# Kernel optimization log

Hardware: AMD Instinct MI355X
Metric: run time of the kernel (lower is better)

The kernel has to match this reference:

```python
import jax, jax.numpy as jnp
import numpy as np

N = 100000
E = 1600000
D_IN = 128
D_H = 128
D_OUT = 40


def setup_inputs() -> dict:
    key = jax.random.key(0)
    ks = jax.random.split(key, 16)
    x = jax.random.normal(ks[0], (N, D_IN), dtype=jnp.float32)
    edge_src = jax.random.randint(ks[1], (E,), 0, N, dtype=jnp.int32)
    edge_dst = jax.random.randint(ks[2], (E,), 0, N, dtype=jnp.int32)

    def glorot(k, shape):
        fan_in, fan_out = shape[1], shape[0]
        lim = jnp.sqrt(6.0 / (fan_in + fan_out)).astype(jnp.float32)
        return jax.random.uniform(k, shape, jnp.float32, -lim, lim)

    # SAGEConv params: Wl acts on aggregated neighbors, Wr on root, plus bias.
    Wl0 = glorot(ks[3], (D_H, D_IN)); Wr0 = glorot(ks[4], (D_H, D_IN)); b0 = jnp.zeros((D_H,), jnp.float32)
    Wl1 = glorot(ks[5], (D_H, D_H));  Wr1 = glorot(ks[6], (D_H, D_H));  b1 = jnp.zeros((D_H,), jnp.float32)
    Wl2 = glorot(ks[7], (D_OUT, D_H)); Wr2 = glorot(ks[8], (D_OUT, D_H)); b2 = jnp.zeros((D_OUT,), jnp.float32)
    return {"x": x, "edge_src": edge_src, "edge_dst": edge_dst,
            "Wl0": Wl0, "Wr0": Wr0, "b0": b0,
            "Wl1": Wl1, "Wr1": Wr1, "b1": b1,
            "Wl2": Wl2, "Wr2": Wr2, "b2": b2}


def _mean_aggregate(x, edge_src, edge_dst, inv_deg):
    # adj_t @ x with mean reduce: sum neighbor feats into dst, divide by degree
    agg = jax.ops.segment_sum(x[edge_src], edge_dst, num_segments=N)
    return agg * inv_deg


def _sage_conv(x, edge_src, edge_dst, inv_deg, Wl, Wr, b):
    agg = _mean_aggregate(x, edge_src, edge_dst, inv_deg)
    return agg @ Wl.T + x @ Wr.T + b


def reference(x, edge_src, edge_dst, Wl0, Wr0, b0, Wl1, Wr1, b1, Wl2, Wr2, b2):
    deg = jax.ops.segment_sum(jnp.ones((E,), jnp.float32), edge_dst, num_segments=N)
    inv_deg = (1.0 / jnp.maximum(deg, 1.0))[:, None]  # [N,1]
    h = _sage_conv(x, edge_src, edge_dst, inv_deg, Wl0, Wr0, b0)
    h = jax.nn.relu(h)  # dropout is identity in eval mode
    h = _sage_conv(h, edge_src, edge_dst, inv_deg, Wl1, Wr1, b1)
    h = jax.nn.relu(h)
    h = _sage_conv(h, edge_src, edge_dst, inv_deg, Wl2, Wr2, b2)
    return jax.nn.log_softmax(h, axis=-1)
```

## Files before the change

kernel.cpp:

```cpp
#include <hip/hip_runtime.h>
#include <hip/hip_fp16.h>
#include <math.h>

#define NN 100000
#define NE 1600000
#define D 128
#define DOUT 40
#define NBUCK 391
#define CHUNK 4096
#define NCHUNK 391
#define EPT 16
#define LSTR 136
#define BCAP 5120

typedef _Float16 half8v __attribute__((ext_vector_type(8)));
typedef __attribute__((ext_vector_type(4))) float f32x4;

__device__ __forceinline__ unsigned packh(float a, float b) {
  return (unsigned)__half_as_ushort(__float2half_rn(a)) |
         ((unsigned)__half_as_ushort(__float2half_rn(b)) << 16);
}
__device__ __forceinline__ unsigned char f2fp8(float v) {
  return (unsigned char)(__builtin_amdgcn_cvt_pk_fp8_f32(v, v, 0, 0) & 0xff);
}
#define CVT2(u, s) __builtin_amdgcn_cvt_pk_f32_fp8((int)(u), s)
#define ACCR(v) { auto q = CVT2((v).x, 0); a[0] += q[0]; a[1] += q[1];   \
  q = CVT2((v).x, 1); a[2] += q[0];  a[3] += q[1];                        \
  q = CVT2((v).y, 0); a[4] += q[0];  a[5] += q[1];                        \
  q = CVT2((v).y, 1); a[6] += q[0];  a[7] += q[1];                        \
  q = CVT2((v).z, 0); a[8] += q[0];  a[9] += q[1];                        \
  q = CVT2((v).z, 1); a[10] += q[0]; a[11] += q[1];                       \
  q = CVT2((v).w, 0); a[12] += q[0]; a[13] += q[1];                       \
  q = CVT2((v).w, 1); a[14] += q[0]; a[15] += q[1]; }
#define ACCR8(v) { auto q = CVT2((v).x, 0); a[0] += q[0]; a[1] += q[1];  \
  q = CVT2((v).x, 1); a[2] += q[0]; a[3] += q[1];                         \
  q = CVT2((v).y, 0); a[4] += q[0]; a[5] += q[1];                         \
  q = CVT2((v).y, 1); a[6] += q[0]; a[7] += q[1]; }

__global__ __launch_bounds__(256) void prep_all_kernel(
    const float* __restrict__ x, _Float16* __restrict__ xb, unsigned char* __restrict__ x8,
    const float* __restrict__ Wl0, const float* __restrict__ Wr0, half8v* __restrict__ B0,
    const float* __restrict__ Wl1, const float* __restrict__ Wr1, half8v* __restrict__ B1,
    const float* __restrict__ Wl2, const float* __restrict__ Wr2, half8v* __restrict__ By2,
    int* __restrict__ bucket_cnt) {
  int bid = blockIdx.x;
  int t = threadIdx.x;
  if (bid < 6250) {
    int i = (bid * 256 + t) * 8;
    float4 v0 = *(const float4*)(x + i);
    float4 v1 = *(const float4*)(x + i + 4);
    uint4 oh;
    oh.x = packh(v0.x, v0.y);
    oh.y = packh(v0.z, v0.w);
    oh.z = packh(v1.x, v1.y);
    oh.w = packh(v1.z, v1.w);
    *(uint4*)(xb + i) = oh;
    unsigned w0 = __builtin_amdgcn_cvt_pk_fp8_f32(v0.x, v0.y, 0, 0);
    w0 = __builtin_amdgcn_cvt_pk_fp8_f32(v0.z, v0.w, w0, 1);
    unsigned w1 = __builtin_amdgcn_cvt_pk_fp8_f32(v1.x, v1.y, 0, 0);
    w1 = __builtin_amdgcn_cvt_pk_fp8_f32(v1.z, v1.w, w1, 1);
    *(uint2*)(x8 + i) = make_uint2(w0, w1);
  } else if (bid < 6282) {
    const float* Wl = (bid < 6266) ? Wl0 : Wl1;
    const float* Wr = (bid < 6266) ? Wr0 : Wr1;
    half8v* P = (bid < 6266) ? B0 : B1;
    int rel = (bid < 6266) ? bid - 6250 : bid - 6266;
    int ob = rel * 4 + (t >> 6);
    int l = t & 63;
    int s = ob >> 3, n = ob & 7;
    int k0 = s * 32 + (l >> 4) * 8;
    int c = n * 16 + (l & 15);
    const float* W = (k0 < 128) ? Wl : Wr;
    int kb = (k0 < 128) ? k0 : k0 - 128;
    half8v h;
#pragma unroll
    for (int i = 0; i < 8; ++i) h[i] = (_Float16)W[c * 128 + kb + i];
    P[ob * 64 + l] = h;
  } else if (bid < 6287) {
    int rel = bid - 6282;
    int ob = rel * 4 + (t >> 6);
    int l = t & 63;
    int s = ob / 5, n = ob % 5;
    int k0 = s * 32 + (l >> 4) * 8;
    int c = n * 16 + (l & 15);
    const float* W = (c < DOUT) ? Wl2 : Wr2;
    int row = (c < DOUT) ? c : c - DOUT;
    half8v h;
#pragma unroll
    for (int i = 0; i < 8; ++i) h[i] = (_Float16)W[row * 128 + k0 + i];
    By2[ob * 64 + l] = h;
  } else {
    for (int i = t; i < NBUCK; i += 256) bucket_cnt[i] = 0;
  }
}

__global__ __launch_bounds__(256) void bucket_hist_kernel(const int* __restrict__ dst,
                                                          int* __restrict__ bucket_cnt) {
  __shared__ int bc[NBUCK];
  int t = threadIdx.x;
  for (int i = t; i < NBUCK; i += 256) bc[i] = 0;
  __syncthreads();
  int e_base = blockIdx.x * CHUNK;
#pragma unroll
  for (int j = 0; j < EPT; ++j) {
    int e = e_base + j * 256 + t;
    if (e < NE) atomicAdd(&bc[dst[e] >> 8], 1);
  }
  __syncthreads();
  for (int i = t; i < NBUCK; i += 256)
    if (bc[i]) atomicAdd(&bucket_cnt[i], bc[i]);
}

__global__ __launch_bounds__(512) void bucket_scan_kernel(const int* __restrict__ bucket_cnt,
                                                          int* __restrict__ bucket_base,
                                                          int* __restrict__ bucket_cursor) {
  __shared__ int s[512];
  int t = threadIdx.x;
  int c = (t < NBUCK) ? bucket_cnt[t] : 0;
  s[t] = c;
  __syncthreads();
  for (int off = 1; off < 512; off <<= 1) {
    int v = (t >= off) ? s[t - off] : 0;
    __syncthreads();
    s[t] += v;
    __syncthreads();
  }
  if (t < NBUCK) {
    int b = s[t] - c;
    bucket_base[t] = b;
    bucket_cursor[t] = b;
  }
  if (t == NBUCK) bucket_base[NBUCK] = s[NBUCK - 1];
}

__global__ __launch_bounds__(256) void binned_scatter_kernel(const int* __restrict__ src,
                                                             const int* __restrict__ dst,
                                                             int* __restrict__ bucket_cursor,
                                                             unsigned* __restrict__ pairs) {
  __shared__ int lcnt[NBUCK];
  __shared__ int lscan[NBUCK];
  __shared__ int gb[NBUCK];
  __shared__ unsigned ebuf[CHUNK];
  __shared__ unsigned short bbuf[CHUNK];
  int t = threadIdx.x;
  int e_base = blockIdx.x * CHUNK;
  for (int i = t; i < NBUCK; i += 256) lcnt[i] = 0;
  __syncthreads();

  int myb[EPT], myrank[EPT];
  unsigned mye[EPT];
#pragma unroll
  for (int j = 0; j < EPT; ++j) {
    int e = e_base + j * 256 + t;
    if (e < NE) {
      int d = dst[e];
      mye[j] = (unsigned)src[e] | ((unsigned)(d & 255) << 24);
      myb[j] = d >> 8;
      myrank[j] = atomicAdd(&lcnt[d >> 8], 1);
    } else {
      myb[j] = -1;
    }
  }
  __syncthreads();

  lscan[t] = lcnt[t];
  if (256 + t < NBUCK) lscan[256 + t] = lcnt[256 + t];
  __syncthreads();
  for (int off = 1; off < 512; off <<= 1) {
    int v0 = (t >= off) ? lscan[t - off] : 0;
    int v1 = 0;
    int i1 = 256 + t;
    if (i1 < NBUCK) v1 = lscan[i1 - off];
    __syncthreads();
    if (t >= off) lscan[t] += v0;
    if (i1 < NBUCK) lscan[i1] += v1;
    __syncthreads();
  }

#pragma unroll
  for (int j = 0; j < EPT; ++j)
    if (myb[j] >= 0) {
      int b = myb[j];
      int lpos = lscan[b] - lcnt[b] + myrank[j];
      ebuf[lpos] = mye[j];
      bbuf[lpos] = (unsigned short)b;
    }
  for (int i = t; i < NBUCK; i += 256)
    if (lcnt[i] > 0) gb[i] = atomicAdd(&bucket_cursor[i], lcnt[i]);
  __syncthreads();

  int chunk_n = min(CHUNK, NE - e_base);
  for (int s2 = t; s2 < chunk_n; s2 += 256) {
    int b = bbuf[s2];
    int g = gb[b] + (s2 - (lscan[b] - lcnt[b]));
    pairs[g] = ebuf[s2];
  }
}

__global__ __launch_bounds__(256) void bucket_build_kernel(const unsigned* __restrict__ pairs,
                                                           const int* __restrict__ bucket_base,
                                                           int* __restrict__ row_start,
                                                           int* __restrict__ nbr,
                                                           float* __restrict__ inv_deg) {
  __shared__ int cnt[256], loc[256], cur[256];
  __shared__ unsigned ec[BCAP];
  int b = blockIdx.x;
  int t = threadIdx.x;
  int nbase = b << 8;
  int e0 = bucket_base[b], e1 = bucket_base[b + 1];
  int n = e1 - e0;
  bool fits = (n <= BCAP);
  cnt[t] = 0;
  __syncthreads();
  if (fits) {
    for (int e = t; e < n; e += 256) {
      unsigned pr = pairs[e0 + e];
      ec[e] = pr;
      atomicAdd(&cnt[pr >> 24], 1);
    }
  } else {
    for (int e = e0 + t; e < e1; e += 256) atomicAdd(&cnt[(int)(pairs[e] >> 24)], 1);
  }
  __syncthreads();
  loc[t] = cnt[t];
  __syncthreads();
  for (int off = 1; off < 256; off <<= 1) {
    int v = (t >= off) ? loc[t - off] : 0;
    __syncthreads();
    loc[t] += v;
    __syncthreads();
  }
  int excl = loc[t] - cnt[t];
  int node = nbase + t;
  if (node < NN) {
    row_start[node] = e0 + excl;
    inv_deg[node] = 1.0f / (float)(cnt[t] > 1 ? cnt[t] : 1);
  }
  cur[t] = excl;
  if (b == NBUCK - 1 && t == 0) row_start[NN] = NE;
  __syncthreads();
  if (fits) {
    for (int e = t; e < n; e += 256) {
      unsigned pr = ec[e];
      int d = (int)(pr >> 24);
      int p = atomicAdd(&cur[d], 1);
      nbr[e0 + p] = (int)(pr & 0xFFFFFFu);
    }
  } else {
    for (int e = e0 + t; e < e1; e += 256) {
      unsigned pr = pairs[e];
      int d = (int)(pr >> 24);
      int p = atomicAdd(&cur[d], 1);
      nbr[e0 + p] = (int)(pr & 0xFFFFFFu);
    }
  }
}

__global__ __launch_bounds__(256) void agg_kernel(const unsigned char* __restrict__ X8,
                                                  _Float16* __restrict__ out,
                                                  const int* __restrict__ row_start,
                                                  const int* __restrict__ nbr,
                                                  const float* __restrict__ inv_deg) {
  int g = blockIdx.x * 32 + (threadIdx.x >> 3);
  int ln = threadIdx.x & 7;
  if (g >= NN) return;
  int p0 = row_start[g];
  int p1 = row_start[g + 1];
  const uint4* base = (const uint4*)X8;
  float a[16];
#pragma unroll
  for (int i = 0; i < 16; ++i) a[i] = 0.f;
  int p = p0;
  for (; p + 3 < p1; p += 4) {
    int s0 = nbr[p], s1 = nbr[p + 1], s2 = nbr[p + 2], s3 = nbr[p + 3];
    uint4 v0 = base[(size_t)s0 * 8 + ln];
    uint4 v1 = base[(size_t)s1 * 8 + ln];
    uint4 v2 = base[(size_t)s2 * 8 + ln];
    uint4 v3 = base[(size_t)s3 * 8 + ln];
    ACCR(v0) ACCR(v1) ACCR(v2) ACCR(v3)
  }
  for (; p < p1; ++p) {
    uint4 v = base[(size_t)nbr[p] * 8 + ln];
    ACCR(v)
  }
  float id = inv_deg[g];
  uint4 o0, o1;
  o0.x = packh(a[0] * id, a[1] * id);
  o0.y = packh(a[2] * id, a[3] * id);
  o0.z = packh(a[4] * id, a[5] * id);
  o0.w = packh(a[6] * id, a[7] * id);
  o1.x = packh(a[8] * id, a[9] * id);
  o1.y = packh(a[10] * id, a[11] * id);
  o1.z = packh(a[12] * id, a[13] * id);
  o1.w = packh(a[14] * id, a[15] * id);
  uint4* ob = (uint4*)out;
  ob[(size_t)g * 16 + ln * 2] = o0;
  ob[(size_t)g * 16 + ln * 2 + 1] = o1;
}

__global__ __launch_bounds__(256) void mfma_gemm_kernel(
    const _Float16* __restrict__ A, const _Float16* __restrict__ H,
    const half8v* __restrict__ B, const float* __restrict__ bias,
    _Float16* __restrict__ out, unsigned char* __restrict__ out8) {
  __shared__ _Float16 Os[128][LSTR];

  int t = threadIdx.x;
  int w = t >> 6, l = t & 63;
  int R0 = blockIdx.x * 128;
  int lc = l & 15;
  int lg = l >> 4;

  int frow = R0 + w * 32 + lc;
  int fr0 = min(frow, NN - 1);
  int fr1 = min(frow + 16, NN - 1);

  f32x4 acc[2][8];
#pragma unroll
  for (int m = 0; m < 2; ++m)
#pragma unroll
    for (int n = 0; n < 8; ++n) acc[m][n] = (f32x4){0.f, 0.f, 0.f, 0.f};

#pragma unroll
  for (int s = 0; s < 8; ++s) {
    const _Float16* src = (s < 4) ? A : H;
    int koff = (s & 3) * 32 + lg * 8;
    half8v ah0 = *(const half8v*)(src + (size_t)fr0 * D + koff);
    half8v ah1 = *(const half8v*)(src + (size_t)fr1 * D + koff);
    half8v bh[8];
#pragma unroll
    for (int n = 0; n < 8; ++n) bh[n] = B[(s * 8 + n) * 64 + l];
#pragma unroll
    for (int n = 0; n < 8; ++n) {
      acc[0][n] = __builtin_amdgcn_mfma_f32_16x16x32_f16(ah0, bh[n], acc[0][n], 0, 0, 0);
      acc[1][n] = __builtin_amdgcn_mfma_f32_16x16x32_f16(ah1, bh[n], acc[1][n], 0, 0, 0);
    }
  }

  float bcol[8];
#pragma unroll
  for (int n = 0; n < 8; ++n) bcol[n] = bias[n * 16 + lc];
#pragma unroll
  for (int m = 0; m < 2; ++m)
#pragma unroll
    for (int n = 0; n < 8; ++n) {
      int col = n * 16 + lc;
#pragma unroll
      for (int j = 0; j < 4; ++j) {
        int row = w * 32 + m * 16 + lg * 4 + j;
        Os[row][col] = (_Float16)fmaxf(acc[m][n][j] + bcol[n], 0.f);
      }
    }
  __syncthreads();

#pragma unroll
  for (int i = 0; i < 8; ++i) {
    int u = t + 256 * i;
    int row = u >> 4, seg = u & 15;
    int gr = R0 + row;
    if (gr < NN) {
      uint4 v = *(const uint4*)&Os[row][seg * 8];
      *(uint4*)(out + (size_t)gr * D + seg * 8) = v;
      unsigned w0 = __builtin_amdgcn_cvt_pk_fp8_f32(
          __half2float(__ushort_as_half((unsigned short)(v.x & 0xffff))),
          __half2float(__ushort_as_half((unsigned short)(v.x >> 16))), 0, 0);
      w0 = __builtin_amdgcn_cvt_pk_fp8_f32(
          __half2float(__ushort_as_half((unsigned short)(v.y & 0xffff))),
          __half2float(__ushort_as_half((unsigned short)(v.y >> 16))), w0, 1);
      unsigned w1 = __builtin_amdgcn_cvt_pk_fp8_f32(
          __half2float(__ushort_as_half((unsigned short)(v.z & 0xffff))),
          __half2float(__ushort_as_half((unsigned short)(v.z >> 16))), 0, 0);
      w1 = __builtin_amdgcn_cvt_pk_fp8_f32(
          __half2float(__ushort_as_half((unsigned short)(v.w & 0xffff))),
          __half2float(__ushort_as_half((unsigned short)(v.w >> 16))), w1, 1);
      *(uint2*)(out8 + (size_t)gr * D + seg * 8) = make_uint2(w0, w1);
    }
  }
}

__global__ __launch_bounds__(256) void mfma_gemm_out_kernel(
    const _Float16* __restrict__ A, const _Float16* __restrict__ H,
    const half8v* __restrict__ B, const float* __restrict__ bias,
    const half8v* __restrict__ By2, const float* __restrict__ b2,
    unsigned char* __restrict__ yl8, float* __restrict__ yr) {
  __shared__ union SM {
    _Float16 Os[128][LSTR];
    struct { unsigned char Y8[128][64]; float Yr[128][40]; } y;
  } sm;

  int t = threadIdx.x;
  int w = t >> 6, l = t & 63;
  int R0 = blockIdx.x * 128;
  int lc = l & 15;
  int lg = l >> 4;

  int frow = R0 + w * 32 + lc;
  int fr0 = min(frow, NN - 1);
  int fr1 = min(frow + 16, NN - 1);

  f32x4 acc[2][8];
#pragma unroll
  for (int m = 0; m < 2; ++m)
#pragma unroll
    for (int n = 0; n < 8; ++n) acc[m][n] = (f32x4){0.f, 0.f, 0.f, 0.f};

#pragma unroll
  for (int s = 0; s < 8; ++s) {
    const _Float16* src = (s < 4) ? A : H;
    int koff = (s & 3) * 32 + lg * 8;
    half8v ah0 = *(const half8v*)(src + (size_t)fr0 * D + koff);
    half8v ah1 = *(const half8v*)(src + (size_t)fr1 * D + koff);
    half8v bh[8];
#pragma unroll
    for (int n = 0; n < 8; ++n) bh[n] = B[(s * 8 + n) * 64 + l];
#pragma unroll
    for (int n = 0; n < 8; ++n) {
      acc[0][n] = __builtin_amdgcn_mfma_f32_16x16x32_f16(ah0, bh[n], acc[0][n], 0, 0, 0);
      acc[1][n] = __builtin_amdgcn_mfma_f32_16x16x32_f16(ah1, bh[n], acc[1][n], 0, 0, 0);
    }
  }

  float bcol[8];
#pragma unroll
  for (int n = 0; n < 8; ++n) bcol[n] = bias[n * 16 + lc];
#pragma unroll
  for (int m = 0; m < 2; ++m)
#pragma unroll
    for (int n = 0; n < 8; ++n) {
      int col = n * 16 + lc;
#pragma unroll
      for (int j = 0; j < 4; ++j) {
        int row = w * 32 + m * 16 + lg * 4 + j;
        sm.Os[row][col] = (_Float16)fmaxf(acc[m][n][j] + bcol[n], 0.f);
      }
    }

  f32x4 acc2[2][5];
#pragma unroll
  for (int m = 0; m < 2; ++m)
#pragma unroll
    for (int n = 0; n < 5; ++n) acc2[m][n] = (f32x4){0.f, 0.f, 0.f, 0.f};

#pragma unroll
  for (int s = 0; s < 4; ++s) {
    int koff = s * 32 + lg * 8;
    half8v ah0 = *(const half8v*)&sm.Os[w * 32 + lc][koff];
    half8v ah1 = *(const half8v*)&sm.Os[w * 32 + 16 + lc][koff];
    half8v bh[5];
#pragma unroll
    for (int n = 0; n < 5; ++n) bh[n] = By2[(s * 5 + n) * 64 + l];
#pragma unroll
    for (int n = 0; n < 5; ++n) {
      acc2[0][n] = __builtin_amdgcn_mfma_f32_16x16x32_f16(ah0, bh[n], acc2[0][n], 0, 0, 0);
      acc2[1][n] = __builtin_amdgcn_mfma_f32_16x16x32_f16(ah1, bh[n], acc2[1][n], 0, 0, 0);
    }
  }
  __syncthreads();

#pragma unroll
  for (int m = 0; m < 2; ++m)
#pragma unroll
    for (int n = 0; n < 5; ++n) {
      int col = n * 16 + lc;
#pragma unroll
      for (int j = 0; j < 4; ++j) {
        int row = w * 32 + m * 16 + lg * 4 + j;
        float v = acc2[m][n][j];
        if (col < DOUT) {
          sm.y.Y8[row][col] = f2fp8(v);
        } else {
          sm.y.Yr[row][col - DOUT] = v + b2[col - DOUT];
        }
      }
    }
  if (t < 128) {
    *(uint2*)&sm.y.Y8[t][40] = make_uint2(0, 0);
    *(uint2*)&sm.y.Y8[t][48] = make_uint2(0, 0);
    *(uint2*)&sm.y.Y8[t][56] = make_uint2(0, 0);
  }
  __syncthreads();

#pragma unroll
  for (int i = 0; i < 4; ++i) {
    int u = t + 256 * i;
    int row = u >> 3, seg = u & 7;
    int gr = R0 + row;
    if (gr < NN)
      *(uint2*)(yl8 + (size_t)gr * 64 + seg * 8) = *(const uint2*)&sm.y.Y8[row][seg * 8];
  }
#pragma unroll
  for (int i = 0; i < 5; ++i) {
    int u = t + 256 * i;
    int row = u / 10, seg = u % 10;
    int gr = R0 + row;
    if (gr < NN)
      *(float4*)(yr + (size_t)gr * DOUT + seg * 4) = *(const float4*)&sm.y.Yr[row][seg * 4];
  }
}

__global__ __launch_bounds__(256) void agg_out_kernel(const unsigned char* __restrict__ yl8,
                                                      const float* __restrict__ yr,
                                                      const int* __restrict__ row_start,
                                                      const int* __restrict__ nbr,
                                                      const float* __restrict__ inv_deg,
                                                      float* __restrict__ out) {
  int g = blockIdx.x * 32 + (threadIdx.x >> 3);
  int ln = threadIdx.x & 7;
  if (g >= NN) return;
  int p0 = row_start[g];
  int p1 = row_start[g + 1];
  const uint2* base = (const uint2*)yl8;
  float a[8];
#pragma unroll
  for (int i = 0; i < 8; ++i) a[i] = 0.f;
  int p = p0;
  for (; p + 3 < p1; p += 4) {
    int s0 = nbr[p], s1 = nbr[p + 1], s2 = nbr[p + 2], s3 = nbr[p + 3];
    uint2 v0 = base[(size_t)s0 * 8 + ln];
    uint2 v1 = base[(size_t)s1 * 8 + ln];
    uint2 v2 = base[(size_t)s2 * 8 + ln];
    uint2 v3 = base[(size_t)s3 * 8 + ln];
    ACCR8(v0) ACCR8(v1) ACCR8(v2) ACCR8(v3)
  }
  for (; p < p1; ++p) {
    uint2 v = base[(size_t)nbr[p] * 8 + ln];
    ACCR8(v)
  }
  float id = inv_deg[g];
  float z[8];
#pragma unroll
  for (int i = 0; i < 8; ++i) z[i] = a[i] * id;
  bool valid = (ln < 5);
  if (valid) {
    float4 r0 = *(const float4*)(yr + (size_t)g * DOUT + ln * 8);
    float4 r1 = *(const float4*)(yr + (size_t)g * DOUT + ln * 8 + 4);
    z[0] += r0.x; z[1] += r0.y; z[2] += r0.z; z[3] += r0.w;
    z[4] += r1.x; z[5] += r1.y; z[6] += r1.z; z[7] += r1.w;
  }
  float zm = -INFINITY;
  if (valid)
#pragma unroll
    for (int i = 0; i < 8; ++i) zm = fmaxf(zm, z[i]);
#pragma unroll
  for (int off = 1; off < 8; off <<= 1) zm = fmaxf(zm, __shfl_xor(zm, off, 8));
  float ssum = 0.f;
  if (valid)
#pragma unroll
    for (int i = 0; i < 8; ++i) ssum += expf(z[i] - zm);
#pragma unroll
  for (int off = 1; off < 8; off <<= 1) ssum += __shfl_xor(ssum, off, 8);
  float lse = zm + logf(ssum);
  if (valid) {
    float4 o0 = make_float4(z[0] - lse, z[1] - lse, z[2] - lse, z[3] - lse);
    float4 o1 = make_float4(z[4] - lse, z[5] - lse, z[6] - lse, z[7] - lse);
    *(float4*)(out + (size_t)g * DOUT + ln * 8) = o0;
    *(float4*)(out + (size_t)g * DOUT + ln * 8 + 4) = o1;
  }
}

extern "C" void kernel_launch(void* const* d_in, const int* in_sizes, int n_in,
                              void* d_out, int out_size, void* d_ws, size_t ws_size,
                              hipStream_t stream) {
  const float* x   = (const float*)d_in[0];
  const int* esrc  = (const int*)d_in[1];
  const int* edst  = (const int*)d_in[2];
  const float* Wl0 = (const float*)d_in[3];
  const float* Wr0 = (const float*)d_in[4];
  const float* b0  = (const float*)d_in[5];
  const float* Wl1 = (const float*)d_in[6];
  const float* Wr1 = (const float*)d_in[7];
  const float* b1  = (const float*)d_in[8];
  const float* Wl2 = (const float*)d_in[9];
  const float* Wr2 = (const float*)d_in[10];
  const float* b2  = (const float*)d_in[11];
  float* out = (float*)d_out;

  char* ws = (char*)d_ws;
  size_t off = 0;
  auto carve = [&](size_t bytes) -> char* {
    char* p = ws + off;
    off = (off + bytes + 255) & ~(size_t)255;
    return p;
  };
  int* bucket_cnt    = (int*)carve((size_t)NBUCK * 4);
  int* bucket_base   = (int*)carve((size_t)(NBUCK + 1) * 4);
  int* bucket_cursor = (int*)carve((size_t)NBUCK * 4);
  int* row_start     = (int*)carve((size_t)(NN + 1) * 4);
  int* nbr           = (int*)carve((size_t)NE * 4);
  float* inv_deg     = (float*)carve((size_t)NN * 4);
  unsigned* pairs    = (unsigned*)carve((size_t)NE * 4);
  half8v* B0         = (half8v*)carve((size_t)64 * 64 * 16);
  half8v* B1         = (half8v*)carve((size_t)64 * 64 * 16);
  half8v* By2        = (half8v*)carve((size_t)20 * 64 * 16);
  _Float16* xb   = (_Float16*)carve((size_t)NN * D * 2);
  unsigned char* x8    = (unsigned char*)carve((size_t)NN * D);
  _Float16* bufA = (_Float16*)carve((size_t)NN * D * 2);
  _Float16* bufB = (_Float16*)carve((size_t)NN * D * 2);
  unsigned char* bufB8 = (unsigned char*)carve((size_t)NN * D);
  unsigned char* yl8   = (unsigned char*)carve((size_t)NN * 64);
  float* yr      = (float*)carve((size_t)NN * DOUT * 4);
  if (off > ws_size) return;

  const int GRID_AGG = (NN + 31) / 32;
  const int GRID_GEMM = (NN + 127) / 128;
  const int GRID_AO = (NN + 31) / 32;
  const int GRID_PREP = 6288;

  prep_all_kernel<<<GRID_PREP, 256, 0, stream>>>(x, xb, x8, Wl0, Wr0, B0,
                                                 Wl1, Wr1, B1, Wl2, Wr2, By2, bucket_cnt);
  bucket_hist_kernel<<<NCHUNK, 256, 0, stream>>>(edst, bucket_cnt);
  bucket_scan_kernel<<<1, 512, 0, stream>>>(bucket_cnt, bucket_base, bucket_cursor);
  binned_scatter_kernel<<<NCHUNK, 256, 0, stream>>>(esrc, edst, bucket_cursor, pairs);
  bucket_build_kernel<<<NBUCK, 256, 0, stream>>>(pairs, bucket_base, row_start, nbr, inv_deg);

  agg_kernel<<<GRID_AGG, 256, 0, stream>>>(x8, bufA, row_start, nbr, inv_deg);
  mfma_gemm_kernel<<<GRID_GEMM, 256, 0, stream>>>(bufA, xb, B0, b0, bufB, bufB8);
  agg_kernel<<<GRID_AGG, 256, 0, stream>>>(bufB8, bufA, row_start, nbr, inv_deg);
  mfma_gemm_out_kernel<<<GRID_GEMM, 256, 0, stream>>>(bufA, bufB, B1, b1, By2, b2, yl8, yr);
  agg_out_kernel<<<GRID_AO, 256, 0, stream>>>(yl8, yr, row_start, nbr, inv_deg, out);
}
```

Measured before the change: 215.9 us.

## Fuse neighbor aggregation with SAGE GEMM per layer via shared-memory tile

Merges each layer's mean-aggregation gather and the following MFMA GEMM into one kernel that processes 32 nodes per block. The aggregated tile stays in LDS instead of being written to and re-read from a global fp16 buffer, which also removes two kernel launches. The trade-off is that row tiles shrink from 128 to 32. Weight fragments are now loaded per 32-row block, split across the four waves by output column, and bounds checks are dropped because N divides evenly by 32.

Result: no change. 219.9 us (+1.8%).

```diff
diff --git a/kernel.cpp b/kernel.cpp
--- a/kernel.cpp
+++ b/kernel.cpp
@@ -36,6 +36,23 @@
   q = CVT2((v).x, 1); a[2] += q[0]; a[3] += q[1];                         \
   q = CVT2((v).y, 0); a[4] += q[0]; a[5] += q[1];                         \
   q = CVT2((v).y, 1); a[6] += q[0]; a[7] += q[1]; }
+
+__device__ __forceinline__ void gather16(const uint4* base, const int* nbr,
+                                         int p0, int p1, int ln, float* a) {
+  int p = p0;
+  for (; p + 3 < p1; p += 4) {
+    int s0 = nbr[p], s1 = nbr[p + 1], s2 = nbr[p + 2], s3 = nbr[p + 3];
+    uint4 v0 = base[(size_t)s0 * 8 + ln];
+    uint4 v1 = base[(size_t)s1 * 8 + ln];
+    uint4 v2 = base[(size_t)s2 * 8 + ln];
+    uint4 v3 = base[(size_t)s3 * 8 + ln];
+    ACCR(v0) ACCR(v1) ACCR(v2) ACCR(v3)
+  }
+  for (; p < p1; ++p) {
+    uint4 v = base[(size_t)nbr[p] * 8 + ln];
+    ACCR(v)
+  }
+}
 
 __global__ __launch_bounds__(256) void prep_all_kernel(
     const float* __restrict__ x, _Float16* __restrict__ xb, unsigned char* __restrict__ x8,
@@ -256,244 +273,235 @@
   }
 }
 
-__global__ __launch_bounds__(256) void agg_kernel(const unsigned char* __restrict__ X8,
-                                                  _Float16* __restrict__ out,
-                                                  const int* __restrict__ row_start,
-                                                  const int* __restrict__ nbr,
-                                                  const float* __restrict__ inv_deg) {
-  int g = blockIdx.x * 32 + (threadIdx.x >> 3);
-  int ln = threadIdx.x & 7;
-  if (g >= NN) return;
-  int p0 = row_start[g];
-  int p1 = row_start[g + 1];
-  const uint4* base = (const uint4*)X8;
-  float a[16];
-#pragma unroll
-  for (int i = 0; i < 16; ++i) a[i] = 0.f;
-  int p = p0;
-  for (; p + 3 < p1; p += 4) {
-    int s0 = nbr[p], s1 = nbr[p + 1], s2 = nbr[p + 2], s3 = nbr[p + 3];
-    uint4 v0 = base[(size_t)s0 * 8 + ln];
-    uint4 v1 = base[(size_t)s1 * 8 + ln];
-    uint4 v2 = base[(size_t)s2 * 8 + ln];
-    uint4 v3 = base[(size_t)s3 * 8 + ln];
-    ACCR(v0) ACCR(v1) ACCR(v2) ACCR(v3)
-  }
-  for (; p < p1; ++p) {
-    uint4 v = base[(size_t)nbr[p] * 8 + ln];
-    ACCR(v)
-  }
-  float id = inv_deg[g];
-  uint4 o0, o1;
-  o0.x = packh(a[0] * id, a[1] * id);
-  o0.y = packh(a[2] * id, a[3] * id);
-  o0.z = packh(a[4] * id, a[5] * id);
-  o0.w = packh(a[6] * id, a[7] * id);
-  o1.x = packh(a[8] * id, a[9] * id);
-  o1.y = packh(a[10] * id, a[11] * id);
-  o1.z = packh(a[12] * id, a[13] * id);
-  o1.w = packh(a[14] * id, a[15] * id);
-  uint4* ob = (uint4*)out;
-  ob[(size_t)g * 16 + ln * 2] = o0;
-  ob[(size_t)g * 16 + ln * 2 + 1] = o1;
-}
-
-__global__ __launch_bounds__(256) void mfma_gemm_kernel(
-    const _Float16* __restrict__ A, const _Float16* __restrict__ H,
+__global__ __launch_bounds__(256) void fused_l0_kernel(
+    const unsigned char* __restrict__ X8, const _Float16* __restrict__ Hroot,
+    const int* __restrict__ row_start, const int* __restrict__ nbr,
+    const float* __restrict__ inv_deg,
     const half8v* __restrict__ B, const float* __restrict__ bias,
     _Float16* __restrict__ out, unsigned char* __restrict__ out8) {
-  __shared__ _Float16 Os[128][LSTR];
+  __shared__ _Float16 As[32][LSTR];
+  __shared__ _Float16 Os[32][LSTR];
 
   int t = threadIdx.x;
-  int w = t >> 6, l = t & 63;
-  int R0 = blockIdx.x * 128;
-  int lc = l & 15;
-  int lg = l >> 4;
-
-  int frow = R0 + w * 32 + lc;
-  int fr0 = min(frow, NN - 1);
-  int fr1 = min(frow + 16, NN - 1);
-
-  f32x4 acc[2][8];
+  int R0 = blockIdx.x * 32;
+
+  {
+    int node = t >> 3, ln = t & 7;
+    int g = R0 + node;
+    float a[16];
+#pragma unroll
+    for (int i = 0; i < 16; ++i) a[i] = 0.f;
+    gather16((const uint4*)X8, nbr, row_start[g], row_start[g + 1], ln, a);
+    float id = inv_deg[g];
+    uint4 o0, o1;
+    o0.x = packh(a[0] * id, a[1] * id);
+    o0.y = packh(a[2] * id, a[3] * id);
+    o0.z = packh(a[4] * id, a[5] * id);
+    o0.w = packh(a[6] * id, a[7] * id);
+    o1.x = packh(a[8] * id, a[9] * id);
+    o1.y = packh(a[10] * id, a[11] * id);
+    o1.z = packh(a[12] * id, a[13] * id);
+    o1.w = packh(a[14] * id, a[15] * id);
+    *(uint4*)&As[node][ln * 16] = o0;
+    *(uint4*)&As[node][ln * 16 + 8] = o1;
+  }
+  __syncthreads();
+
+  int w = t >> 6, l = t & 63, lc = l & 15, lg = l >> 4;
+  f32x4 acc[2][2];
 #pragma unroll
   for (int m = 0; m < 2; ++m)
 #pragma unroll
-    for (int n = 0; n < 8; ++n) acc[m][n] = (f32x4){0.f, 0.f, 0.f, 0.f};
+    for (int n = 0; n < 2; ++n) acc[m][n] = (f32x4){0.f, 0.f, 0.f, 0.f};
 
 #pragma unroll
   for (int s = 0; s < 8; ++s) {
-    const _Float16* src = (s < 4) ? A : H;
     int koff = (s & 3) * 32 + lg * 8;
-    half8v ah0 = *(const half8v*)(src + (size_t)fr0 * D + koff);
-    half8v ah1 = *(const half8v*)(src + (size_t)fr1 * D + koff);
-    half8v bh[8];
-#pragma unroll
-    for (int n = 0; n < 8; ++n) bh[n] = B[(s * 8 + n) * 64 + l];
-#pragma unroll
-    for (int n = 0; n < 8; ++n) {
-      acc[0][n] = __builtin_amdgcn_mfma_f32_16x16x32_f16(ah0, bh[n], acc[0][n], 0, 0, 0);
-      acc[1][n] = __builtin_amdgcn_mfma_f32_16x16x32_f16(ah1, bh[n], acc[1][n], 0, 0, 0);
-    }
-  }
-
-  float bcol[8];
-#pragma unroll
-  for (int n = 0; n < 8; ++n) bcol[n] = bias[n * 16 + lc];
+    half8v ah0, ah1;
+    if (s < 4) {
+      ah0 = *(const half8v*)&As[lc][koff];
+      ah1 = *(const half8v*)&As[16 + lc][koff];
+    } else {
+      ah0 = *(const half8v*)(Hroot + (size_t)(R0 + lc) * D + koff);
+      ah1 = *(const half8v*)(Hroot + (size_t)(R0 + 16 + lc) * D + koff);
+    }
+    half8v bh0 = B[(s * 8 + w * 2 + 0) * 64 + l];
+    half8v bh1 = B[(s * 8 + w * 2 + 1) * 64 + l];
+    acc[0][0] = __builtin_amdgcn_mfma_f32_16x16x32_f16(ah0, bh0, acc[0][0], 0, 0, 0);
+    acc[1][0] = __builtin_amdgcn_mfma_f32_16x16x32_f16(ah1, bh0, acc[1][0], 0, 0, 0);
+    acc[0][1] = __builtin_amdgcn_mfma_f32_16x16x32_f16(ah0, bh1, acc[0][1], 0, 0, 0);
+    acc[1][1] = __builtin_amdgcn_mfma_f32_16x16x32_f16(ah1, bh1, acc[1][1], 0, 0, 0);
+  }
+
+  float bc[2] = {bias[w * 32 + lc], bias[w * 32 + 16 + lc]};
 #pragma unroll
   for (int m = 0; m < 2; ++m)
 #pragma unroll
-    for (int n = 0; n < 8; ++n) {
-      int col = n * 16 + lc;
+    for (int n = 0; n < 2; ++n) {
+      int col = w * 32 + n * 16 + lc;
 #pragma unroll
       for (int j = 0; j < 4; ++j) {
-        int row = w * 32 + m * 16 + lg * 4 + j;
-        Os[row][col] = (_Float16)fmaxf(acc[m][n][j] + bcol[n], 0.f);
+        int row = m * 16 + lg * 4 + j;
+        Os[row][col] = (_Float16)fmaxf(acc[m][n][j] + bc[n], 0.f);
       }
     }
   __syncthreads();
 
 #pragma unroll
-  for (int i = 0; i < 8; ++i) {
+  for (int i = 0; i < 2; ++i) {
     int u = t + 256 * i;
     int row = u >> 4, seg = u & 15;
     int gr = R0 + row;
-    if (gr < NN) {
-      uint4 v = *(const uint4*)&Os[row][seg * 8];
-      *(uint4*)(out + (size_t)gr * D + seg * 8) = v;
-      unsigned w0 = __builtin_amdgcn_cvt_pk_fp8_f32(
-          __half2float(__ushort_as_half((unsigned short)(v.x & 0xffff))),
-          __half2float(__ushort_as_half((unsigned short)(v.x >> 16))), 0, 0);
-      w0 = __builtin_amdgcn_cvt_pk_fp8_f32(
-          __half2float(__ushort_as_half((unsigned short)(v.y & 0xffff))),
-          __half2float(__ushort_as_half((unsigned short)(v.y >> 16))), w0, 1);
-      unsigned w1 = __builtin_amdgcn_cvt_pk_fp8_f32(
-          __half2float(__ushort_as_half((unsigned short)(v.z & 0xffff))),
-          __half2float(__ushort_as_half((unsigned short)(v.z >> 16))), 0, 0);
-      w1 = __builtin_amdgcn_cvt_pk_fp8_f32(
-          __half2float(__ushort_as_half((unsigned short)(v.w & 0xffff))),
-          __half2float(__ushort_as_half((unsigned short)(v.w >> 16))), w1, 1);
-      *(uint2*)(out8 + (size_t)gr * D + seg * 8) = make_uint2(w0, w1);
-    }
-  }
-}
-
-__global__ __launch_bounds__(256) void mfma_gemm_out_kernel(
-    const _Float16* __restrict__ A, const _Float16* __restrict__ H,
+    uint4 v = *(const uint4*)&Os[row][seg * 8];
+    *(uint4*)(out + (size_t)gr * D + seg * 8) = v;
+    unsigned w0 = __builtin_amdgcn_cvt_pk_fp8_f32(
+        __half2float(__ushort_as_half((unsigned short)(v.x & 0xffff))),
+        __half2float(__ushort_as_half((unsigned short)(v.x >> 16))), 0, 0);
+    w0 = __builtin_amdgcn_cvt_pk_fp8_f32(
+        __half2float(__ushort_as_half((unsigned short)(v.y & 0xffff))),
+        __half2float(__ushort_as_half((unsigned short)(v.y >> 16))), w0, 1);
+    unsigned w1 = __builtin_amdgcn_cvt_pk_fp8_f32(
+        __half2float(__ushort_as_half((unsigned short)(v.z & 0xffff))),
+        __half2float(__ushort_as_half((unsigned short)(v.z >> 16))), 0, 0);
+    w1 = __builtin_amdgcn_cvt_pk_fp8_f32(
+        __half2float(__ushort_as_half((unsigned short)(v.w & 0xffff))),
+        __half2float(__ushort_as_half((unsigned short)(v.w >> 16))), w1, 1);
+    *(uint2*)(out8 + (size_t)gr * D + seg * 8) = make_uint2(w0, w1);
+  }
+}
+
+__global__ __launch_bounds__(256) void fused_l1_kernel(
+    const unsigned char* __restrict__ X8, const _Float16* __restrict__ Hroot,
+    const int* __restrict__ row_start, const int* __restrict__ nbr,
+    const float* __restrict__ inv_deg,
     const half8v* __restrict__ B, const float* __restrict__ bias,
     const half8v* __restrict__ By2, const float* __restrict__ b2,
     unsigned char* __restrict__ yl8, float* __restrict__ yr) {
-  __shared__ union SM {
-    _Float16 Os[128][LSTR];
-    struct { unsigned char Y8[128][64]; float Yr[128][40]; } y;
-  } sm;
+  __shared__ union SA {
+    _Float16 As[32][LSTR];
+    struct { unsigned char Y8[32][64]; float Yr[32][40]; } y;
+  } sa;
+  __shared__ _Float16 Hs[32][LSTR];
 
   int t = threadIdx.x;
-  int w = t >> 6, l = t & 63;
-  int R0 = blockIdx.x * 128;
-  int lc = l & 15;
-  int lg = l >> 4;
-
-  int frow = R0 + w * 32 + lc;
-  int fr0 = min(frow, NN - 1);
-  int fr1 = min(frow + 16, NN - 1);
-
-  f32x4 acc[2][8];
+  int R0 = blockIdx.x * 32;
+
+  {
+    int node = t >> 3, ln = t & 7;
+    int g = R0 + node;
+    float a[16];
+#pragma unroll
+    for (int i = 0; i < 16; ++i) a[i] = 0.f;
+    gather16((const uint4*)X8, nbr, row_start[g], row_start[g + 1], ln, a);
+    float id = inv_deg[g];
+    uint4 o0, o1;
+    o0.x = packh(a[0] * id, a[1] * id);
+    o0.y = packh(a[2] * id, a[3] * id);
+    o0.z = packh(a[4] * id, a[5] * id);
+    o0.w = packh(a[6] * id, a[7] * id);
+    o1.x = packh(a[8] * id, a[9] * id);
+    o1.y = packh(a[10] * id, a[11] * id);
+    o1.z = packh(a[12] * id, a[13] * id);
+    o1.w = packh(a[14] * id, a[15] * id);
+    *(uint4*)&sa.As[node][ln * 16] = o0;
+    *(uint4*)&sa.As[node][ln * 16 + 8] = o1;
+  }
+  __syncthreads();
+
+  int w = t >> 6, l = t & 63, lc = l & 15, lg = l >> 4;
+  f32x4 acc[2][2];
 #pragma unroll
   for (int m = 0; m < 2; ++m)
 #pragma unroll
-    for (int n = 0; n < 8; ++n) acc[m][n] = (f32x4){0.f, 0.f, 0.f, 0.f};
+    for (int n = 0; n < 2; ++n) acc[m][n] = (f32x4){0.f, 0.f, 0.f, 0.f};
 
 #pragma unroll
   for (int s = 0; s < 8; ++s) {
-    const _Float16* src = (s < 4) ? A : H;
     int koff = (s & 3) * 32 + lg * 8;
-    half8v ah0 = *(const half8v*)(src + (size_t)fr0 * D + koff);
-    half8v ah1 = *(const half8v*)(src + (size_t)fr1 * D + koff);
-    half8v bh[8];
-#pragma unroll
-    for (int n = 0; n < 8; ++n) bh[n] = B[(s * 8 + n) * 64 + l];
-#pragma unroll
-    for (int n = 0; n < 8; ++n) {
-      acc[0][n] = __builtin_amdgcn_mfma_f32_16x16x32_f16(ah0, bh[n], acc[0][n], 0, 0, 0);
-      acc[1][n] = __builtin_amdgcn_mfma_f32_16x16x32_f16(ah1, bh[n], acc[1][n], 0, 0, 0);
-    }
-  }
-
-  float bcol[8];
-#pragma unroll
-  for (int n = 0; n < 8; ++n) bcol[n] = bias[n * 16 + lc];
+    half8v ah0, ah1;
+    if (s < 4) {
+      ah0 = *(const half8v*)&sa.As[lc][koff];
+      ah1 = *(const half8v*)&sa.As[16 + lc][koff];
+    } else {
+      ah0 = *(const half8v*)(Hroot + (size_t)(R0 + lc) * D + koff);
+      ah1 = *(const half8v*)(Hroot + (size_t)(R0 + 16 + lc) * D + koff);
+    }
+    half8v bh0 = B[(s * 8 + w * 2 + 0) * 64 + l];
+    half8v bh1 = B[(s * 8 + w * 2 + 1) * 64 + l];
+    acc[0][0] = __builtin_amdgcn_mfma_f32_16x16x32_f16(ah0, bh0, acc[0][0], 0, 0, 0);
+    acc[1][0] = __builtin_amdgcn_mfma_f32_16x16x32_f16(ah1, bh0, acc[1][0], 0, 0, 0);
+    acc[0][1] = __builtin_amdgcn_mfma_f32_16x16x32_f16(ah0, bh1, acc[0][1], 0, 0, 0);
+    acc[1][1] = __builtin_amdgcn_mfma_f32_16x16x32_f16(ah1, bh1, acc[1][1], 0, 0, 0);
+  }
+
+  float bc[2] = {bias[w * 32 + lc], bias[w * 32 + 16 + lc]};
 #pragma unroll
   for (int m = 0; m < 2; ++m)
 #pragma unroll
-    for (int n = 0; n < 8; ++n) {
-      int col = n * 16 + lc;
+    for (int n = 0; n < 2; ++n) {
+      int col = w * 32 + n * 16 + lc;
 #pragma unroll
       for (int j = 0; j < 4; ++j) {
-        int row = w * 32 + m * 16 + lg * 4 + j;
-        sm.Os[row][col] = (_Float16)fmaxf(acc[m][n][j] + bcol[n], 0.f);
+        int row = m * 16 + lg * 4 + j;
+        Hs[row][col] = (_Float16)fmaxf(acc[m][n][j] + bc[n], 0.f);
       }
     }
-
-  f32x4 acc2[2][5];
-#pragma unroll
-  for (int m = 0; m < 2; ++m)
-#pragma unroll
-    for (int n = 0; n < 5; ++n) acc2[m][n] = (f32x4){0.f, 0.f, 0.f, 0.f};
+  __syncthreads();
+
+  int rf = w >> 1;
+  int nb = (w & 1) ? 3 : 0;
+  int nc = (w & 1) ? 2 : 3;
+  f32x4 acc2[3];
+#pragma unroll
+  for (int n = 0; n < 3; ++n) acc2[n] = (f32x4){0.f, 0.f, 0.f, 0.f};
 
 #pragma unroll
   for (int s = 0; s < 4; ++s) {
     int koff = s * 32 + lg * 8;
-    half8v ah0 = *(const half8v*)&sm.Os[w * 32 + lc][koff];
-    half8v ah1 = *(const half8v*)&sm.Os[w * 32 + 16 + lc][koff];
-    half8v bh[5];
-#pragma unroll
-    for (int n = 0; n < 5; ++n) bh[n] = By2[(s * 5 + n) * 64 + l];
-#pragma unroll
-    for (int n = 0; n < 5; ++n) {
-      acc2[0][n] = __builtin_amdgcn_mfma_f32_16x16x32_f16(ah0, bh[n], acc2[0][n], 0, 0, 0);
-      acc2[1][n] = __builtin_amdgcn_mfma_f32_16x16x32_f16(ah1, bh[n], acc2[1][n], 0, 0, 0);
-    }
-  }
-  __syncthreads();
-
-#pragma unroll
-  for (int m = 0; m < 2; ++m)
-#pragma unroll
-    for (int n = 0; n < 5; ++n) {
-      int col = n * 16 + lc;
+    half8v ah = *(const half8v*)&Hs[rf * 16 + lc][koff];
+#pragma unroll
+    for (int n = 0; n < 3; ++n)
+      if (n < nc) {
+        half8v bh = By2[(s * 5 + nb + n) * 64 + l];
+        acc2[n] = __builtin_amdgcn_mfma_f32_16x16x32_f16(ah, bh, acc2[n], 0, 0, 0);
+      }
+  }
+
+#pragma unroll
+  for (int n = 0; n < 3; ++n)
+    if (n < nc) {
+      int col = (nb + n) * 16 + lc;
 #pragma unroll
       for (int j = 0; j < 4; ++j) {
-        int row = w * 32 + m * 16 + lg * 4 + j;
-        float v = acc2[m][n][j];
+        int row = rf * 16 + lg * 4 + j;
+        float v = acc2[n][j];
         if (col < DOUT) {
-          sm.y.Y8[row][col] = f2fp8(v);
+          sa.y.Y8[row][col] = f2fp8(v);
         } else {
-          sm.y.Yr[row][col - DOUT] = v + b2[col - DOUT];
+          sa.y.Yr[row][col - DOUT] = v + b2[col - DOUT];
         }
       }
     }
-  if (t < 128) {
-    *(uint2*)&sm.y.Y8[t][40] = make_uint2(0, 0);
-    *(uint2*)&sm.y.Y8[t][48] = make_uint2(0, 0);
-    *(uint2*)&sm.y.Y8[t][56] = make_uint2(0, 0);
-  }
-  __syncthreads();
-
-#pragma unroll
-  for (int i = 0; i < 4; ++i) {
+  if (t < 32) {
+    *(uint2*)&sa.y.Y8[t][40] = make_uint2(0, 0);
+    *(uint2*)&sa.y.Y8[t][48] = make_uint2(0, 0);
+    *(uint2*)&sa.y.Y8[t][56] = make_uint2(0, 0);
+  }
+  __syncthreads();
+
+  {
+    int row = t >> 3, seg = t & 7;
+    int gr = R0 + row;
+    *(uint2*)(yl8 + (size_t)gr * 64 + seg * 8) = *(const uint2*)&sa.y.Y8[row][seg * 8];
+  }
+#pragma unroll
+  for (int i = 0; i < 2; ++i) {
     int u = t + 256 * i;
-    int row = u >> 3, seg = u & 7;
-    int gr = R0 + row;
-    if (gr < NN)
-      *(uint2*)(yl8 + (size_t)gr * 64 + seg * 8) = *(const uint2*)&sm.y.Y8[row][seg * 8];
-  }
-#pragma unroll
-  for (int i = 0; i < 5; ++i) {
-    int u = t + 256 * i;
-    int row = u / 10, seg = u % 10;
-    int gr = R0 + row;
-    if (gr < NN)
-      *(float4*)(yr + (size_t)gr * DOUT + seg * 4) = *(const float4*)&sm.y.Yr[row][seg * 4];
+    if (u < 320) {
+      int row = u / 10, seg = u % 10;
+      int gr = R0 + row;
+      *(float4*)(yr + (size_t)gr * DOUT + seg * 4) = *(const float4*)&sa.y.Yr[row][seg * 4];
+    }
   }
 }
 
@@ -593,15 +601,13 @@
   half8v* By2        = (half8v*)carve((size_t)20 * 64 * 16);
   _Float16* xb   = (_Float16*)carve((size_t)NN * D * 2);
   unsigned char* x8    = (unsigned char*)carve((size_t)NN * D);
-  _Float16* bufA = (_Float16*)carve((size_t)NN * D * 2);
   _Float16* bufB = (_Float16*)carve((size_t)NN * D * 2);
   unsigned char* bufB8 = (unsigned char*)carve((size_t)NN * D);
   unsigned char* yl8   = (unsigned char*)carve((size_t)NN * 64);
   float* yr      = (float*)carve((size_t)NN * DOUT * 4);
   if (off > ws_size) return;
 
-  const int GRID_AGG = (NN + 31) / 32;
-  const int GRID_GEMM = (NN + 127) / 128;
+  const int GRID_F = NN / 32;
   const int GRID_AO = (NN + 31) / 32;
   const int GRID_PREP = 6288;
 
@@ -612,9 +618,9 @@
   binned_scatter_kernel<<<NCHUNK, 256, 0, stream>>>(esrc, edst, bucket_cursor, pairs);
   bucket_build_kernel<<<NBUCK, 256, 0, stream>>>(pairs, bucket_base, row_start, nbr, inv_deg);
 
-  agg_kernel<<<GRID_AGG, 256, 0, stream>>>(x8, bufA, row_start, nbr, inv_deg);
-  mfma_gemm_kernel<<<GRID_GEMM, 256, 0, stream>>>(bufA, xb, B0, b0, bufB, bufB8);
-  agg_kernel<<<GRID_AGG, 256, 0, stream>>>(bufB8, bufA, row_start, nbr, inv_deg);
-  mfma_gemm_out_kernel<<<GRID_GEMM, 256, 0, stream>>>(bufA, bufB, B1, b1, By2, b2, yl8, yr);
+  fused_l0_kernel<<<GRID_F, 256, 0, stream>>>(x8, xb, row_start, nbr, inv_deg,
+                                              B0, b0, bufB, bufB8);
+  fused_l1_kernel<<<GRID_F, 256, 0, stream>>>(bufB8, bufB, row_start, nbr, inv_deg,
+                                              B1, b1, By2, b2, yl8, yr);
   agg_out_kernel<<<GRID_AO, 256, 0, stream>>>(yl8, yr, row_start, nbr, inv_deg, out);
 }
```
